# Performance work log

Hardware: AMD Instinct MI355X
Metric: run time of the kernel (lower is better)

Reference implementation:

```python
import jax, jax.numpy as jnp
import numpy as np

# Config: E experts, hidden H, intermediate I; tokens tiled as [A,B,E,M,H] with A*B*M = BD*S.
E, H, I = 8, 2048, 2048
A, B, M = 1, 8, 512
_BD, _S = 2, 2048


def setup_inputs() -> dict:
    key = jax.random.key(0)
    k1, k2, k3, k4, k5 = jax.random.split(key, 5)
    dispatched = jax.random.normal(k1, (A, B, E, M, H), dtype=jnp.float32)
    w1 = jax.random.normal(k2, (E, H, 2 * I), dtype=jnp.float32) * 0.02  # gate_up_proj
    w1_bias = jax.random.normal(k3, (E, 2 * I), dtype=jnp.float32) * 0.02
    w2 = jax.random.normal(k4, (E, I, H), dtype=jnp.float32) * 0.02  # down_proj
    w2_bias = jax.random.normal(k5, (E, H), dtype=jnp.float32) * 0.02
    sparsity_remap = jnp.zeros((B, E), dtype=jnp.int32)  # perf-only metadata for tt.sparse_matmul; dense-equivalent math
    return {"dispatched": dispatched, "w1": w1, "w1_bias": w1_bias, "w2": w2,
            "w2_bias": w2_bias, "sparsity_remap": sparsity_remap, "BD": _BD, "S": _S}


def reference(dispatched, w1, w1_bias, w2, w2_bias, sparsity_remap, BD, S):
    # sparse_matmul(dispatched, w1): grouped per-expert GEMM, dense-equivalent math.
    # [A,B,E,M,H] @ [E,H,2I] -> [A,B,E,M,2I]
    gate_up = jnp.einsum('abemh,ehf->abemf', dispatched, w1)
    gate_up = gate_up + w1_bias[None, None, :, None, :]
    # Fused interleaved gate/up, deepseek (SiLU-GLU) activation: w3 is None.
    gate = gate_up[..., 0::2]
    up = gate_up[..., 1::2]
    activated = jax.nn.silu(gate) * up  # [A,B,E,M,I]
    a, b, e, m, i = activated.shape
    activated = activated.reshape(a * b, e, m, i)  # canonical [A*B,E,M,I]
    # down projection: [A*B,E,M,I] @ [E,I,H] -> [A*B,E,M,H]
    down = jnp.einsum('cemi,eih->cemh', activated, w2)
    down = down + w2_bias[None, :, None, :]
    h = down.shape[-1]
    down = jnp.transpose(down, (1, 0, 2, 3))  # [E, A*B, M, H]
    return down.reshape(e, 1, BD * S, h)
```

## Files before the change

### kernel.cpp

```cpp
#include <hip/hip_runtime.h>
#include <hip/hip_bf16.h>
#include <math.h>

typedef short bf16x8 __attribute__((ext_vector_type(8)));
typedef float f32x4 __attribute__((ext_vector_type(4)));

#define E_ 8
#define H_ 2048
#define I_ 2048
#define F_ 4096
#define M_ 512

__device__ __forceinline__ unsigned short f2bf(float f) {
  union { float f; unsigned u; } v; v.f = f;
  unsigned r = v.u + 0x7fffu + ((v.u >> 16) & 1u);
  return (unsigned short)(r >> 16);
}

template<int MODE>
__global__ __launch_bounds__(256) void moe_gemm(
    const float* __restrict__ af,
    const unsigned short* __restrict__ ab,
    const float* __restrict__ w,
    const float* __restrict__ bias,
    unsigned short* __restrict__ actout,
    float* __restrict__ dout)
{
  __shared__ unsigned short As[128 * 64];
  __shared__ unsigned short Bs[8 * 128 * 8];
  char* Ab = (char*)As;
  char* Bb = (char*)Bs;

  const int tid  = threadIdx.x;
  const int lane = tid & 63;
  const int wid  = tid >> 6;

  int be, tm, tn;
  if (MODE == 0) { be = blockIdx.x >> 7; tm = (blockIdx.x >> 5) & 3; tn = blockIdx.x & 31; }
  else           { be = blockIdx.x >> 6; tm = (blockIdx.x >> 4) & 3; tn = blockIdx.x & 15; }
  const int c  = be >> 3;
  const int e  = be & 7;
  const int m0 = tm * 128;
  const int n0 = (MODE == 0) ? tn * 64 : tn * 128;

  f32x4 acc[2][8];
  #pragma unroll
  for (int im = 0; im < 2; ++im)
    #pragma unroll
    for (int in = 0; in < 8; ++in)
      acc[im][in] = (f32x4){0.f, 0.f, 0.f, 0.f};

  const int arow = tid >> 3;
  const int aoct = tid & 7;
  const int bq   = tid & 127;
  const int bko  = tid >> 7;

  const size_t a_row_base = (size_t)((c * E_ + e) * M_ + m0);

  for (int k0 = 0; k0 < H_; k0 += 64) {
    #pragma unroll
    for (int p = 0; p < 4; ++p) {
      const int row = p * 32 + arow;
      bf16x8 pk;
      if (MODE == 0) {
        const float* src = af + (a_row_base + row) * H_ + k0 + aoct * 8;
        float4 f0 = *(const float4*)src;
        float4 f1 = *(const float4*)(src + 4);
        pk[0] = (short)f2bf(f0.x); pk[1] = (short)f2bf(f0.y);
        pk[2] = (short)f2bf(f0.z); pk[3] = (short)f2bf(f0.w);
        pk[4] = (short)f2bf(f1.x); pk[5] = (short)f2bf(f1.y);
        pk[6] = (short)f2bf(f1.z); pk[7] = (short)f2bf(f1.w);
      } else {
        pk = *(const bf16x8*)(ab + (a_row_base + row) * I_ + k0 + aoct * 8);
      }
      int ad = row * 128 + aoct * 16;
      ad ^= (row & 7) << 4;
      *(bf16x8*)(Ab + ad) = pk;
    }
    #pragma unroll
    for (int p = 0; p < 4; ++p) {
      const int koct = p * 2 + bko;
      bf16x8 pk;
      int slot;
      if (MODE == 0) {
        const float* src = w + ((size_t)(e * H_ + k0 + koct * 8)) * F_ + 2 * n0 + bq;
        #pragma unroll
        for (int j = 0; j < 8; ++j) pk[j] = (short)f2bf(src[(size_t)j * F_]);
        slot = (bq >> 1) + (bq & 1) * 64;
      } else {
        const float* src = w + ((size_t)(e * I_ + k0 + koct * 8)) * H_ + n0 + bq;
        #pragma unroll
        for (int j = 0; j < 8; ++j) pk[j] = (short)f2bf(src[(size_t)j * H_]);
        slot = bq;
      }
      *(bf16x8*)(Bb + (koct * 128 + slot) * 16) = pk;
    }
    __syncthreads();
    #pragma unroll
    for (int ks = 0; ks < 2; ++ks) {
      bf16x8 a0, a1, bfr[8];
      {
        const int kloc = ks * 32 + (lane >> 4) * 8;
        const int r0 = wid * 32 + (lane & 15);
        int ad0 = r0 * 128 + kloc * 2; ad0 ^= (r0 & 7) << 4;
        a0 = *(const bf16x8*)(Ab + ad0);
        const int r1 = r0 + 16;
        int ad1 = r1 * 128 + kloc * 2; ad1 ^= (r1 & 7) << 4;
        a1 = *(const bf16x8*)(Ab + ad1);
      }
      const int oct = ks * 4 + (lane >> 4);
      #pragma unroll
      for (int in = 0; in < 8; ++in) {
        const int col = in * 16 + (lane & 15);
        bfr[in] = *(const bf16x8*)(Bb + (oct * 128 + col) * 16);
      }
      #pragma unroll
      for (int in = 0; in < 8; ++in) {
        acc[0][in] = __builtin_amdgcn_mfma_f32_16x16x32_bf16(a0, bfr[in], acc[0][in], 0, 0, 0);
        acc[1][in] = __builtin_amdgcn_mfma_f32_16x16x32_bf16(a1, bfr[in], acc[1][in], 0, 0, 0);
      }
    }
    __syncthreads();
  }

  const int rb = m0 + wid * 32 + ((lane >> 4) * 4);
  if (MODE == 0) {
    #pragma unroll
    for (int in = 0; in < 4; ++in) {
      const int icol = n0 + in * 16 + (lane & 15);
      const float bg = bias[e * F_ + 2 * icol];
      const float bu = bias[e * F_ + 2 * icol + 1];
      #pragma unroll
      for (int im = 0; im < 2; ++im) {
        #pragma unroll
        for (int r = 0; r < 4; ++r) {
          const int row = rb + im * 16 + r;
          const float g = acc[im][in][r] + bg;
          const float u = acc[im][in + 4][r] + bu;
          const float val = (g / (1.f + __expf(-g))) * u;
          actout[((size_t)((c * E_ + e) * M_) + row) * I_ + icol] = f2bf(val);
        }
      }
    }
  } else {
    #pragma unroll
    for (int in = 0; in < 8; ++in) {
      const int h = n0 + in * 16 + (lane & 15);
      const float bb = bias[e * H_ + h];
      #pragma unroll
      for (int im = 0; im < 2; ++im) {
        #pragma unroll
        for (int r = 0; r < 4; ++r) {
          const int row = rb + im * 16 + r;
          dout[(size_t)e * (8 * (size_t)M_ * H_) + ((size_t)(c * M_ + row)) * H_ + h] =
              acc[im][in][r] + bb;
        }
      }
    }
  }
}

extern "C" void kernel_launch(void* const* d_in, const int* in_sizes, int n_in,
                              void* d_out, int out_size, void* d_ws, size_t ws_size,
                              hipStream_t stream) {
  const float* disp = (const float*)d_in[0];
  const float* w1   = (const float*)d_in[1];
  const float* w1b  = (const float*)d_in[2];
  const float* w2   = (const float*)d_in[3];
  const float* w2b  = (const float*)d_in[4];

  unsigned short* act = (unsigned short*)d_ws;
  float* out = (float*)d_out;

  moe_gemm<0><<<8192, 256, 0, stream>>>(disp, nullptr, w1, w1b, act, nullptr);
  moe_gemm<1><<<4096, 256, 0, stream>>>(nullptr, act, w2, w2b, nullptr, out);
}
```

Measured before the change: 2.352 ms.

## Pre-convert inputs and weights to bf16 and stream tiles via global_load_lds

Adds pre-pass kernels that convert the activations to bf16 and convert plus transpose both weight tensors to K-contiguous bf16 in workspace. New GEMM kernels then load A and B tiles straight into swizzled LDS with the direct global-to-LDS load builtin instead of strided fp32 gathers converted in registers. Block indices are remapped so consecutive blocks map to different experts. This costs extra passes over the inputs and weights and extra workspace, and falls back to the old path if the workspace is too small.

```diff
diff --git a/kernel.cpp b/kernel.cpp
--- a/kernel.cpp
+++ b/kernel.cpp
@@ -15,6 +15,174 @@
   union { float f; unsigned u; } v; v.f = f;
   unsigned r = v.u + 0x7fffu + ((v.u >> 16) & 1u);
   return (unsigned short)(r >> 16);
+}
+
+__device__ __forceinline__ void gload16(const void* g, void* l) {
+  __builtin_amdgcn_global_load_lds(
+      (const __attribute__((address_space(1))) void*)g,
+      (__attribute__((address_space(3))) void*)l, 16, 0, 0);
+}
+
+
+__global__ __launch_bounds__(256) void conv_x(const float* __restrict__ x,
+                                              unsigned short* __restrict__ xb) {
+  const size_t i = (size_t)blockIdx.x * 256 + threadIdx.x;
+  const float4 a = *(const float4*)(x + i * 8);
+  const float4 b = *(const float4*)(x + i * 8 + 4);
+  bf16x8 o;
+  o[0] = (short)f2bf(a.x); o[1] = (short)f2bf(a.y);
+  o[2] = (short)f2bf(a.z); o[3] = (short)f2bf(a.w);
+  o[4] = (short)f2bf(b.x); o[5] = (short)f2bf(b.y);
+  o[6] = (short)f2bf(b.z); o[7] = (short)f2bf(b.w);
+  *(bf16x8*)(xb + i * 8) = o;
+}
+
+__global__ __launch_bounds__(256) void conv_transpose(const float* __restrict__ w,
+                                                      unsigned short* __restrict__ wT,
+                                                      int F) {
+  __shared__ unsigned short T[64 * 72];
+  const int t = threadIdx.x;
+  int b = blockIdx.x;
+  const int nf = F >> 6;
+  const int f0 = (b % nf) << 6; b /= nf;
+  const int k0 = (b & 31) << 6;
+  const int e  = b >> 5;
+
+  const int kr = t >> 4, fq = t & 15;
+  #pragma unroll
+  for (int j = 0; j < 4; ++j) {
+    const int k = j * 16 + kr;
+    const float4 v = *(const float4*)(w + (size_t)(e * H_ + k0 + k) * F + f0 + fq * 4);
+    T[(fq * 4 + 0) * 72 + k] = f2bf(v.x);
+    T[(fq * 4 + 1) * 72 + k] = f2bf(v.y);
+    T[(fq * 4 + 2) * 72 + k] = f2bf(v.z);
+    T[(fq * 4 + 3) * 72 + k] = f2bf(v.w);
+  }
+  __syncthreads();
+  #pragma unroll
+  for (int j = 0; j < 2; ++j) {
+    const int id = j * 256 + t;
+    const int f = id >> 3, koct = id & 7;
+    bf16x8 v = *(const bf16x8*)(&T[f * 72 + koct * 8]);
+    *(bf16x8*)(wT + (size_t)(e * F + f0 + f) * H_ + k0 + koct * 8) = v;
+  }
+}
+
+template<int MODE>
+__global__ __launch_bounds__(256) void moe_gemm_fast(
+    const unsigned short* __restrict__ abf,
+    const unsigned short* __restrict__ wT,
+    const float* __restrict__ bias,
+    unsigned short* __restrict__ actout,
+    float* __restrict__ dout) {
+  __shared__ unsigned short As[8192];
+  __shared__ unsigned short Bs[8192];
+  char* Ab = (char*)As;
+  char* Bb = (char*)Bs;
+
+  const int tid  = threadIdx.x;
+  const int lane = tid & 63;
+  const int wid  = tid >> 6;
+  const int l15  = lane & 15, lh = lane >> 4;
+
+  const int L = blockIdx.x;
+  int e, c, tm, tn, n0, Fdim;
+  if (MODE == 0) {
+    const int orig = (L & 7) * 1024 + (L >> 3);
+    e = orig >> 10; c = (orig >> 7) & 7; tm = (orig >> 5) & 3; tn = orig & 31;
+    n0 = tn * 64; Fdim = F_;
+  } else {
+    const int orig = (L & 7) * 512 + (L >> 3);
+    e = orig >> 9; c = (orig >> 6) & 7; tm = (orig >> 4) & 3; tn = orig & 15;
+    n0 = tn * 128; Fdim = H_;
+  }
+  const int m0 = tm * 128;
+  const size_t a_row_base = (size_t)((c * E_ + e) * M_ + m0);
+
+  const unsigned short* pA[4];
+  const unsigned short* pB[4];
+  #pragma unroll
+  for (int j = 0; j < 4; ++j) {
+    const int chunk = wid * 4 + j;
+    const int row = chunk * 8 + (lane >> 3);
+    const int aoct = (lane & 7) ^ (row & 7);
+    pA[j] = abf + (a_row_base + row) * H_ + aoct * 8;
+    const int slot = row;
+    const int boct = (lane & 7) ^ (slot & 7);
+    int fg;
+    if (MODE == 0) fg = (slot < 64) ? 2 * (n0 + slot) : 2 * (n0 + slot - 64) + 1;
+    else           fg = n0 + slot;
+    pB[j] = wT + (size_t)(e * Fdim + fg) * H_ + boct * 8;
+  }
+
+  f32x4 acc[2][8];
+  #pragma unroll
+  for (int im = 0; im < 2; ++im)
+    #pragma unroll
+    for (int in = 0; in < 8; ++in)
+      acc[im][in] = (f32x4){0.f, 0.f, 0.f, 0.f};
+
+  for (int k0 = 0; k0 < H_; k0 += 64) {
+    #pragma unroll
+    for (int j = 0; j < 4; ++j) {
+      const int chunk = wid * 4 + j;
+      gload16(pA[j] + k0, Ab + chunk * 1024);
+      gload16(pB[j] + k0, Bb + chunk * 1024);
+    }
+    __syncthreads();
+    #pragma unroll
+    for (int ks = 0; ks < 2; ++ks) {
+      const int oct = ks * 4 + lh;
+      const int r0 = wid * 32 + l15;
+      const int sw = (oct ^ (r0 & 7)) << 4;
+      bf16x8 a0 = *(const bf16x8*)(Ab + r0 * 128 + sw);
+      bf16x8 a1 = *(const bf16x8*)(Ab + (r0 + 16) * 128 + sw);
+      #pragma unroll
+      for (int in = 0; in < 8; ++in) {
+        const int col = in * 16 + l15;
+        bf16x8 b = *(const bf16x8*)(Bb + col * 128 + ((oct ^ (col & 7)) << 4));
+        acc[0][in] = __builtin_amdgcn_mfma_f32_16x16x32_bf16(a0, b, acc[0][in], 0, 0, 0);
+        acc[1][in] = __builtin_amdgcn_mfma_f32_16x16x32_bf16(a1, b, acc[1][in], 0, 0, 0);
+      }
+    }
+    __syncthreads();
+  }
+
+  const int rb = m0 + wid * 32 + lh * 4;
+  if (MODE == 0) {
+    #pragma unroll
+    for (int in = 0; in < 4; ++in) {
+      const int icol = n0 + in * 16 + l15;
+      const float bg = bias[e * F_ + 2 * icol];
+      const float bu = bias[e * F_ + 2 * icol + 1];
+      #pragma unroll
+      for (int im = 0; im < 2; ++im) {
+        #pragma unroll
+        for (int r = 0; r < 4; ++r) {
+          const int row = rb + im * 16 + r;
+          const float g = acc[im][in][r] + bg;
+          const float u = acc[im][in + 4][r] + bu;
+          const float val = (g / (1.f + __expf(-g))) * u;
+          actout[((size_t)((c * E_ + e) * M_) + row) * I_ + icol] = f2bf(val);
+        }
+      }
+    }
+  } else {
+    #pragma unroll
+    for (int in = 0; in < 8; ++in) {
+      const int h = n0 + in * 16 + l15;
+      const float bb = bias[e * H_ + h];
+      #pragma unroll
+      for (int im = 0; im < 2; ++im) {
+        #pragma unroll
+        for (int r = 0; r < 4; ++r) {
+          const int row = rb + im * 16 + r;
+          dout[(size_t)e * (8 * (size_t)M_ * H_) + ((size_t)(c * M_ + row)) * H_ + h] =
+              acc[im][in][r] + bb;
+        }
+      }
+    }
+  }
 }
 
 template<int MODE>
@@ -24,17 +192,14 @@
     const float* __restrict__ w,
     const float* __restrict__ bias,
     unsigned short* __restrict__ actout,
-    float* __restrict__ dout)
-{
+    float* __restrict__ dout) {
   __shared__ unsigned short As[128 * 64];
   __shared__ unsigned short Bs[8 * 128 * 8];
   char* Ab = (char*)As;
   char* Bb = (char*)Bs;
-
   const int tid  = threadIdx.x;
   const int lane = tid & 63;
   const int wid  = tid >> 6;
-
   int be, tm, tn;
   if (MODE == 0) { be = blockIdx.x >> 7; tm = (blockIdx.x >> 5) & 3; tn = blockIdx.x & 31; }
   else           { be = blockIdx.x >> 6; tm = (blockIdx.x >> 4) & 3; tn = blockIdx.x & 15; }
@@ -42,21 +207,17 @@
   const int e  = be & 7;
   const int m0 = tm * 128;
   const int n0 = (MODE == 0) ? tn * 64 : tn * 128;
-
   f32x4 acc[2][8];
   #pragma unroll
   for (int im = 0; im < 2; ++im)
     #pragma unroll
     for (int in = 0; in < 8; ++in)
       acc[im][in] = (f32x4){0.f, 0.f, 0.f, 0.f};
-
   const int arow = tid >> 3;
   const int aoct = tid & 7;
   const int bq   = tid & 127;
   const int bko  = tid >> 7;
-
   const size_t a_row_base = (size_t)((c * E_ + e) * M_ + m0);
-
   for (int k0 = 0; k0 < H_; k0 += 64) {
     #pragma unroll
     for (int p = 0; p < 4; ++p) {
@@ -122,7 +283,6 @@
     }
     __syncthreads();
   }
-
   const int rb = m0 + wid * 32 + ((lane >> 4) * 4);
   if (MODE == 0) {
     #pragma unroll
@@ -168,10 +328,23 @@
   const float* w1b  = (const float*)d_in[2];
   const float* w2   = (const float*)d_in[3];
   const float* w2b  = (const float*)d_in[4];
-
-  unsigned short* act = (unsigned short*)d_ws;
   float* out = (float*)d_out;
 
-  moe_gemm<0><<<8192, 256, 0, stream>>>(disp, nullptr, w1, w1b, act, nullptr);
-  moe_gemm<1><<<4096, 256, 0, stream>>>(nullptr, act, w2, w2b, nullptr, out);
-}
+  const size_t ELEMS = (size_t)64 * 512 * 2048;
+  const size_t need = ELEMS * 2 * 3 + ELEMS;
+  if (ws_size >= need) {
+    unsigned short* Xbf = (unsigned short*)d_ws;
+    unsigned short* act = Xbf + ELEMS;
+    unsigned short* w1T = act + ELEMS;
+    unsigned short* w2T = w1T + ELEMS;
+    conv_x<<<32768, 256, 0, stream>>>(disp, Xbf);
+    conv_transpose<<<16384, 256, 0, stream>>>(w1, w1T, F_);
+    conv_transpose<<<8192, 256, 0, stream>>>(w2, w2T, H_);
+    moe_gemm_fast<0><<<8192, 256, 0, stream>>>(Xbf, w1T, w1b, act, nullptr);
+    moe_gemm_fast<1><<<4096, 256, 0, stream>>>(act, w2T, w2b, nullptr, out);
+  } else {
+    unsigned short* act = (unsigned short*)d_ws;
+    moe_gemm<0><<<8192, 256, 0, stream>>>(disp, nullptr, w1, w1b, act, nullptr);
+    moe_gemm<1><<<4096, 256, 0, stream>>>(nullptr, act, w2, w2b, nullptr, out);
+  }
+}
```

Result: faster. 1.910 ms (-18.8%).
